# Optimization experiments

Hardware: AMD Instinct MI355X
Metric: run time of the kernel (lower is better)

## Reference

```python
import jax, jax.numpy as jnp
import numpy as np

TEMPERATURE = 0.5  # NT-Xent temperature (SimCLR default in SACLR)
NEG_INF = -1e9


def ntxent(zi, zj, temperature=TEMPERATURE):
    """SimCLR NT-Xent between two views zi, zj of shape [B, D]."""
    B = zi.shape[0]
    z = jnp.concatenate([zi, zj], axis=0)                      # [2B, D]
    z = z / (jnp.linalg.norm(z, axis=1, keepdims=True) + 1e-8)  # cosine sim
    sim = (z @ z.T) / temperature                              # [2B, 2B]
    n = 2 * B
    sim = jnp.where(jnp.eye(n, dtype=bool), NEG_INF, sim)      # mask self
    labels = jnp.concatenate([jnp.arange(B) + B, jnp.arange(B)])
    logp = jax.nn.log_softmax(sim, axis=1)
    return -jnp.mean(logp[jnp.arange(n), labels])


def setup_inputs() -> dict:
    key = jax.random.key(0)
    k1, k2, k3 = jax.random.split(key, 3)
    B, D, W, H, CA = 512, 256, 14, 14, 8
    return {
        "global_feature": jax.random.normal(k1, (B, D), dtype=jnp.float32),
        "att": jax.random.uniform(k2, (B, CA, W, H), dtype=jnp.float32),
        "outputs": jax.random.normal(k3, (B, D, W, H), dtype=jnp.float32),
    }


def reference(global_feature, att, outputs):
    # attention = sum over attention-map channel, shape [B, W, H]
    attention = jnp.sum(att, axis=1)
    B, D, W, H = outputs.shape
    P = W * H
    # Flatten spatial positions in the same (i over W, j over H) row-major order
    # as the original nested python loops.
    local_feats = jnp.transpose(outputs, (2, 3, 0, 1)).reshape(P, B, D)   # [P, B, D]
    local_atts = jnp.transpose(attention, (1, 2, 0)).reshape(P, B)        # [P, B]

    # Faithful quirk of the original: global_feature is re-softmaxed at every
    # spatial position (it is reassigned inside the loop), so carry it in a scan.
    def step(g, xs):
        lf, la = xs
        g = jax.nn.softmax(g, axis=1)          # repeated softmax on global
        lf = jax.nn.softmax(lf, axis=1)        # softmax on local feature
        l = ntxent(lf, g) * jnp.mean(la) / P   # weighted NT-Xent term
        return g, l

    _, losses = jax.lax.scan(step, global_feature, (local_feats, local_atts))
    return jnp.sum(losses)
```

## Files before the change

### kernel.cpp

```cpp
#include <hip/hip_runtime.h>

#define B_   512
#define D_   256
#define P_   196
#define N2B  1024

#define CSCALE 1.69864364f
#define LN2    0.69314718f
#define T2L    2.8853900817779268f

typedef __attribute__((ext_vector_type(8))) short short8;
typedef __attribute__((ext_vector_type(4))) float f32x4;
typedef unsigned int u32;

#define LDSP(x) ((__attribute__((address_space(3))) u32*)(x))
#define GLBP(x) ((const __attribute__((address_space(1))) u32*)(x))

__device__ unsigned short g_Z[(size_t)P_ * N2B * D_];
__device__ float g_rowps[(size_t)P_ * 8 * N2B];
__device__ float g_pp2[P_ * 4];
__device__ float g_mApart[128 * P_];
__device__ float g_dscale[(size_t)B_ * P_];
__device__ float g_partials[P_];

static __device__ const unsigned char TROW36[36] = {
  0,0,0,0,0,0,0,0, 1,1,1,1,1,1,1, 2,2,2,2,2,2, 3,3,3,3,3, 4,4,4,4, 5,5,5, 6,6, 7};
static __device__ const unsigned char TCOL36[36] = {
  0,1,2,3,4,5,6,7, 1,2,3,4,5,6,7, 2,3,4,5,6,7, 3,4,5,6,7, 4,5,6,7, 5,6,7, 6,7, 7};

static __device__ inline unsigned short f2bf(float f) {
    union { float f; unsigned int u; } v; v.f = f;
    unsigned int u = v.u;
    return (unsigned short)((u + 0x7fffu + ((u >> 16) & 1u)) >> 16);
}
static __device__ inline float bf2f(unsigned short h) {
    union { unsigned int u; float f; } v; v.u = ((unsigned int)h) << 16;
    return v.f;
}
static __device__ inline float wave_sum(float v) {
    for (int off = 32; off > 0; off >>= 1) v += __shfl_xor(v, off, 64);
    return v;
}

template<int CTRL>
static __device__ inline float dpp_add_step(float v) {
    int t = __builtin_amdgcn_update_dpp(0, __float_as_int(v), CTRL, 0xf, 0xf, true);
    return v + __int_as_float(t);
}
static __device__ inline float row16_sum(float v) {
    v = dpp_add_step<0xB1>(v);
    v = dpp_add_step<0x4E>(v);
    v = dpp_add_step<0x141>(v);
    v = dpp_add_step<0x140>(v);
    return v;
}

__global__ __launch_bounds__(256) void prep12_kernel(const float* __restrict__ gf,
                                                     const float* __restrict__ att,
                                                     const float* __restrict__ outs) {
    int blk = blockIdx.x, t = threadIdx.x;

    if (blk < 32) {
        int wv = t >> 6, lane = t & 63;
        int rw = lane >> 4, lr = lane & 15;
        int b = blk * 16 + wv * 4 + rw;
        const float4* gfr = (const float4*)(gf + (size_t)b * D_);
        float g[16], e[16];
        {
            float4 q0 = gfr[lr], q1 = gfr[lr + 16], q2 = gfr[lr + 32], q3 = gfr[lr + 48];
            g[0]=q0.x; g[1]=q0.y; g[2]=q0.z; g[3]=q0.w;
            g[4]=q1.x; g[5]=q1.y; g[6]=q1.z; g[7]=q1.w;
            g[8]=q2.x; g[9]=q2.y; g[10]=q2.z; g[11]=q2.w;
            g[12]=q3.x; g[13]=q3.y; g[14]=q3.z; g[15]=q3.w;
        }
        for (int p = 0; p < P_; ++p) {
            float s1 = 0.0f, s2 = 0.0f;
#pragma unroll
            for (int i = 0; i < 16; ++i) {
                e[i] = __expf(g[i]);
                s1 += e[i];
                s2 = fmaf(e[i], e[i], s2);
            }
            s1 = row16_sum(s1);
            s2 = row16_sum(s2);
            float isq = rsqrtf(s2) * CSCALE;
            float inv = 1.0f / s1;
            unsigned short* zr = g_Z + ((size_t)p * N2B + B_ + b) * D_;
#pragma unroll
            for (int c = 0; c < 4; ++c) {
                ushort4 o;
                o.x = f2bf(e[c * 4 + 0] * isq);
                o.y = f2bf(e[c * 4 + 1] * isq);
                o.z = f2bf(e[c * 4 + 2] * isq);
                o.w = f2bf(e[c * 4 + 3] * isq);
                *(ushort4*)(zr + c * 64 + lr * 4) = o;
            }
#pragma unroll
            for (int i = 0; i < 16; ++i) g[i] = e[i] * inv;
        }
    } else if (blk < 544) {
        int b = blk - 32;
        if (t < P_) {
            const float* src = outs + (size_t)b * (D_ * P_) + t;
            float s = 0.0f;
#pragma unroll 8
            for (int d = 0; d < 256; ++d) s += exp2f(src[(size_t)d * P_] * T2L);
            g_dscale[(size_t)b * P_ + t] = rsqrtf(s) * CSCALE;
        }
    } else {
        int bk = blk - 544;
        if (t < P_) {
            float acc = 0.0f;
            const float* base = att + (size_t)bk * 32 * P_ + t;
            for (int r = 0; r < 32; ++r) acc += base[(size_t)r * P_];
            g_mApart[bk * P_ + t] = acc;
        }
    }
}

__global__ __launch_bounds__(256) void prep2_kernel(const float* __restrict__ outs) {
    __shared__ unsigned short vt[128 * 202];
    __shared__ float ss[P_];
    int blk = blockIdx.x, t = threadIdx.x;
    int b = blk >> 1, dh = blk & 1;
    const float4* src4 = (const float4*)(outs + (size_t)b * (D_ * P_) + dh * (128 * P_));
    for (int idx = t; idx < 6272; idx += 256) {
        int d = idx / 49, c = idx - d * 49;
        float4 v = src4[idx];
        unsigned short* dst = vt + d * 202 + c * 4;
        ushort2 a, bb;
        a.x = f2bf(v.x); a.y = f2bf(v.y); bb.x = f2bf(v.z); bb.y = f2bf(v.w);
        *(ushort2*)dst = a; *(ushort2*)(dst + 2) = bb;
    }
    if (t < P_) ss[t] = g_dscale[(size_t)b * P_ + t];
    __syncthreads();
    int w = t >> 6, l = t & 63;
    for (int i = 0; i < 49; ++i) {
        int p = w * 49 + i;
        float v0 = bf2f(vt[(2 * l) * 202 + p]);
        float v1 = bf2f(vt[(2 * l + 1) * 202 + p]);
        float sc = ss[p];
        ushort2 o;
        o.x = f2bf(__expf(v0) * sc);
        o.y = f2bf(__expf(v1) * sc);
        *(ushort2*)(g_Z + ((size_t)p * N2B + b) * D_ + dh * 128 + 2 * l) = o;
    }
}

template<int MODE>
static __device__ inline void do_epi(const f32x4 acc[4][4], float psum[4][4], float pcs[4],
                                     float& pp, int wdiag, int lr, int r4) {
#pragma unroll
    for (int i = 0; i < 4; ++i) {
#pragma unroll
        for (int j = 0; j < 4; ++j) {
#pragma unroll
            for (int r = 0; r < 4; ++r) {
                float a = acc[i][j][r];
                float e = exp2f(a);
                if (MODE == 1) {
                    if (wdiag && i == j) e = (r4 + r == lr) ? 0.0f : e;
                }
                psum[i][r] += e;
                pcs[j] += e;
                if (MODE == 2) {
                    if (wdiag && i == j && (r4 + r == lr)) pp += a * LN2;
                }
            }
        }
    }
}

__global__ __launch_bounds__(256, 4) void sim_kernel() {
    __shared__ __align__(16) unsigned short As[128 * 64];
    __shared__ __align__(16) unsigned short Bs[128 * 64];
    __shared__ float combuf[512];
    __shared__ float ppred[4];

    int lin0 = blockIdx.x;
    int xcd = lin0 & 7, slot = lin0 >> 3;
    int lin = xcd * 882 + slot;
    int p = lin / 36;
    int t36 = lin - p * 36;
    int trow = TROW36[t36], tcol = TCOL36[t36];
    bool DIAG = (trow == tcol);
    bool PART = (trow < 4) && (tcol == trow + 4);

    int tid = threadIdx.x;
    int wv = tid >> 6, lane = tid & 63;
    int wr = wv >> 1, wc = wv & 1;
    int lr = lane & 15;
    int lk16 = (lane >> 4) * 16;
    bool skipw = DIAG && (wv == 2);

    const char* zb = (const char*)g_Z + (size_t)p * ((size_t)N2B * D_ * 2);
    const char* gA = zb + (size_t)trow * (128 * 512);
    const char* gB = zb + (size_t)tcol * (128 * 512);
    int lsub = (lane >> 3) * 512 + (((lane & 7) ^ (lane >> 3)) << 4);

    f32x4 acc[4][4];
#pragma unroll
    for (int i = 0; i < 4; ++i)
#pragma unroll
        for (int j = 0; j < 4; ++j)
            acc[i][j] = (f32x4){0.0f, 0.0f, 0.0f, 0.0f};

    const char* BsR = DIAG ? (const char*)As : (const char*)Bs;

    for (int ko = 0; ko < 4; ++ko) {
#pragma unroll
        for (int it = 0; it < 4; ++it) {
            int s = it * 4 + wv;
            int go = s * 4096 + ko * 128 + lsub;
            __builtin_amdgcn_global_load_lds(GLBP(gA + go), LDSP((char*)As + s * 1024), 16, 0, 0);
            if (!DIAG)
                __builtin_amdgcn_global_load_lds(GLBP(gB + go), LDSP((char*)Bs + s * 1024), 16, 0, 0);
        }
        __syncthreads();
        if (!skipw) {
#pragma unroll
            for (int ks = 0; ks < 2; ++ks) {
                int kswz = (ks * 64 + lk16) ^ ((lr & 7) << 4);
                short8 a[4], b[4];
#pragma unroll
                for (int i = 0; i < 4; ++i) {
                    a[i] = *(const short8*)((const char*)As + (wr * 64 + i * 16 + lr) * 128 + kswz);
                    b[i] = *(const short8*)(BsR + (wc * 64 + i * 16 + lr) * 128 + kswz);
                }
#pragma unroll
                for (int i = 0; i < 4; ++i)
#pragma unroll
                    for (int j = 0; j < 4; ++j)
                        acc[i][j] = __builtin_amdgcn_mfma_f32_16x16x32_bf16(a[i], b[j], acc[i][j], 0, 0, 0);
            }
        }
        __syncthreads();
    }

    int wdiag = (wr == wc);
    int r4 = (lane >> 4) * 4;
    float psum[4][4];
    float pcs[4] = {0.0f, 0.0f, 0.0f, 0.0f};
    float pp = 0.0f;
#pragma unroll
    for (int i = 0; i < 4; ++i)
#pragma unroll
        for (int r = 0; r < 4; ++r) psum[i][r] = 0.0f;

    if (!skipw) {
        if (DIAG)      do_epi<1>(acc, psum, pcs, pp, wdiag, lr, r4);
        else if (PART) do_epi<2>(acc, psum, pcs, pp, wdiag, lr, r4);
        else           do_epi<0>(acc, psum, pcs, pp, wdiag, lr, r4);
    }

    float* rowbuf = combuf;
    float* colbuf = combuf + 256;
    if (!skipw) {
#pragma unroll
        for (int i = 0; i < 4; ++i)
#pragma unroll
            for (int r = 0; r < 4; ++r) {
                float ps = psum[i][r];
                ps += __shfl_xor(ps, 1, 64);
                ps += __shfl_xor(ps, 2, 64);
                ps += __shfl_xor(ps, 4, 64);
                ps += __shfl_xor(ps, 8, 64);
                if (lr == 0) rowbuf[wc * 128 + wr * 64 + i * 16 + r4 + r] = ps;
            }
    }
    if (!DIAG) {
#pragma unroll
        for (int j = 0; j < 4; ++j) {
            float pc = pcs[j];
            pc += __shfl_xor(pc, 16, 64);
            pc += __shfl_xor(pc, 32, 64);
            if (lane < 16) colbuf[wr * 128 + wc * 64 + j * 16 + lane] = pc;
        }
    } else if (wv == 1) {
#pragma unroll
        for (int j = 0; j < 4; ++j) {
            float pc = pcs[j];
            pc += __shfl_xor(pc, 16, 64);
            pc += __shfl_xor(pc, 32, 64);
            if (lane < 16) rowbuf[64 + j * 16 + lane] = pc;
        }
    }
    if (PART) {
        float pw = wave_sum(pp);
        if (lane == 0) ppred[wv] = pw;
    }
    __syncthreads();

    if (tid < 128) {
        float v = rowbuf[tid] + rowbuf[128 + tid];
        g_rowps[((size_t)p * 8 + tcol) * N2B + trow * 128 + tid] = v;
    } else if (!DIAG) {
        int x = tid - 128;
        float v = colbuf[x] + colbuf[128 + x];
        g_rowps[((size_t)p * 8 + trow) * N2B + tcol * 128 + x] = v;
    }
    if (PART && tid == 0)
        g_pp2[p * 4 + trow] = 2.0f * (ppred[0] + ppred[1] + ppred[2] + ppred[3]);
}

__global__ __launch_bounds__(256) void rowreduce_kernel() {
    int p = blockIdx.x, t = threadIdx.x;
    const float* base = g_rowps + (size_t)p * 8 * N2B;
    float s = 0.0f;
    for (int r = t; r < N2B; r += 256) {
        float S = 0.0f;
#pragma unroll
        for (int k = 0; k < 8; ++k) S += base[(size_t)k * N2B + r];
        s += __logf(S);
    }
    s = wave_sum(s);
    __shared__ float red[4];
    int wv = t >> 6, lane = t & 63;
    if (lane == 0) red[wv] = s;
    __syncthreads();
    if (t == 0) {
        float tot = red[0] + red[1] + red[2] + red[3];
        float pp = g_pp2[p * 4 + 0] + g_pp2[p * 4 + 1] + g_pp2[p * 4 + 2] + g_pp2[p * 4 + 3];
        float ma = 0.0f;
        for (int k = 0; k < 128; ++k) ma += g_mApart[k * P_ + p];
        g_partials[p] = (tot - pp) * (ma * (1.0f / B_));
    }
}

__global__ __launch_bounds__(256) void final_kernel(float* __restrict__ out) {
    int t = threadIdx.x;
    float s = (t < P_) ? g_partials[t] : 0.0f;
    s = wave_sum(s);
    __shared__ float red[4];
    int wv = t >> 6, lane = t & 63;
    if (lane == 0) red[wv] = s;
    __syncthreads();
    if (t == 0) out[0] = (red[0] + red[1] + red[2] + red[3]) * (1.0f / ((float)N2B * (float)P_));
}

extern "C" void kernel_launch(void* const* d_in, const int* in_sizes, int n_in,
                              void* d_out, int out_size, void* d_ws, size_t ws_size,
                              hipStream_t stream) {
    const float* gf   = (const float*)d_in[0];
    const float* att  = (const float*)d_in[1];
    const float* outs = (const float*)d_in[2];
    float* out = (float*)d_out;

    hipLaunchKernelGGL(prep12_kernel, dim3(672), dim3(256), 0, stream, gf, att, outs);
    hipLaunchKernelGGL(prep2_kernel, dim3(B_ * 2), dim3(256), 0, stream, outs);
    hipLaunchKernelGGL(sim_kernel, dim3(P_ * 36), dim3(256), 0, stream);
    hipLaunchKernelGGL(rowreduce_kernel, dim3(P_), dim3(256), 0, stream);
    hipLaunchKernelGGL(final_kernel, dim3(1), dim3(256), 0, stream, out);
}
```

Measured before the change: 353.8 us.

## Double-buffer LDS tiles in sim kernel and parallelize attention-mean reduction

Splits the sim kernel's K loop into a two-stage LDS double buffer. Global-to-LDS loads for step k+2 are issued while MFMAs consume step k, with explicit vmcnt waits and barriers, and occupancy is lowered to 2 blocks per CU to fit the doubled shared memory. Diagonal tiles now load B into their own buffer as well, which adds redundant traffic. Separately, the rowreduce kernel replaces a 128-iteration serial loop on thread 0 with a wave-level parallel sum.

```diff
diff --git a/kernel.cpp b/kernel.cpp
--- a/kernel.cpp
+++ b/kernel.cpp
@@ -171,9 +171,9 @@
     }
 }
 
-__global__ __launch_bounds__(256, 4) void sim_kernel() {
-    __shared__ __align__(16) unsigned short As[128 * 64];
-    __shared__ __align__(16) unsigned short Bs[128 * 64];
+__global__ __launch_bounds__(256, 2) void sim_kernel() {
+    __shared__ __align__(16) unsigned short As[2][8192];
+    __shared__ __align__(16) unsigned short Bs[2][8192];
     __shared__ float combuf[512];
     __shared__ float ppred[4];
 
@@ -205,37 +205,57 @@
         for (int j = 0; j < 4; ++j)
             acc[i][j] = (f32x4){0.0f, 0.0f, 0.0f, 0.0f};
 
-    const char* BsR = DIAG ? (const char*)As : (const char*)Bs;
-
-    for (int ko = 0; ko < 4; ++ko) {
-#pragma unroll
-        for (int it = 0; it < 4; ++it) {
-            int s = it * 4 + wv;
-            int go = s * 4096 + ko * 128 + lsub;
-            __builtin_amdgcn_global_load_lds(GLBP(gA + go), LDSP((char*)As + s * 1024), 16, 0, 0);
-            if (!DIAG)
-                __builtin_amdgcn_global_load_lds(GLBP(gB + go), LDSP((char*)Bs + s * 1024), 16, 0, 0);
-        }
-        __syncthreads();
-        if (!skipw) {
-#pragma unroll
-            for (int ks = 0; ks < 2; ++ks) {
-                int kswz = (ks * 64 + lk16) ^ ((lr & 7) << 4);
-                short8 a[4], b[4];
-#pragma unroll
-                for (int i = 0; i < 4; ++i) {
-                    a[i] = *(const short8*)((const char*)As + (wr * 64 + i * 16 + lr) * 128 + kswz);
-                    b[i] = *(const short8*)(BsR + (wc * 64 + i * 16 + lr) * 128 + kswz);
-                }
-#pragma unroll
-                for (int i = 0; i < 4; ++i)
-#pragma unroll
-                    for (int j = 0; j < 4; ++j)
-                        acc[i][j] = __builtin_amdgcn_mfma_f32_16x16x32_bf16(a[i], b[j], acc[i][j], 0, 0, 0);
-            }
-        }
-        __syncthreads();
-    }
+#define STAGE(KO, BUF) \
+    _Pragma("unroll") \
+    for (int it = 0; it < 4; ++it) { \
+        int s = it * 4 + wv; \
+        int go = s * 4096 + (KO) * 128 + lsub; \
+        __builtin_amdgcn_global_load_lds(GLBP(gA + go), LDSP((char*)As[BUF] + s * 1024), 16, 0, 0); \
+        __builtin_amdgcn_global_load_lds(GLBP(gB + go), LDSP((char*)Bs[BUF] + s * 1024), 16, 0, 0); \
+    }
+
+    STAGE(0, 0)
+    STAGE(1, 1)
+
+#define SIM_ITER(KO, VMS) { \
+    asm volatile("s_waitcnt vmcnt(" VMS ")" ::: "memory"); \
+    __builtin_amdgcn_sched_barrier(0); \
+    __builtin_amdgcn_s_barrier(); \
+    __builtin_amdgcn_sched_barrier(0); \
+    short8 a[2][4], b[2][4]; \
+    if (!skipw) { \
+        _Pragma("unroll") \
+        for (int ks = 0; ks < 2; ++ks) { \
+            int kswz = (ks * 64 + lk16) ^ ((lr & 7) << 4); \
+            _Pragma("unroll") \
+            for (int i = 0; i < 4; ++i) { \
+                a[ks][i] = *(const short8*)((const char*)As[(KO) & 1] + (wr * 64 + i * 16 + lr) * 128 + kswz); \
+                b[ks][i] = *(const short8*)((const char*)Bs[(KO) & 1] + (wc * 64 + i * 16 + lr) * 128 + kswz); \
+            } \
+        } \
+    } \
+    asm volatile("s_waitcnt lgkmcnt(0)" ::: "memory"); \
+    __builtin_amdgcn_sched_barrier(0); \
+    __builtin_amdgcn_s_barrier(); \
+    __builtin_amdgcn_sched_barrier(0); \
+    if ((KO) + 2 < 4) { STAGE((KO) + 2, (KO) & 1) } \
+    if (!skipw) { \
+        _Pragma("unroll") \
+        for (int ks = 0; ks < 2; ++ks) \
+            _Pragma("unroll") \
+            for (int i = 0; i < 4; ++i) \
+                _Pragma("unroll") \
+                for (int j = 0; j < 4; ++j) \
+                    acc[i][j] = __builtin_amdgcn_mfma_f32_16x16x32_bf16(a[ks][i], b[ks][j], acc[i][j], 0, 0, 0); \
+    } \
+}
+
+    SIM_ITER(0, "8")
+    SIM_ITER(1, "8")
+    SIM_ITER(2, "8")
+    SIM_ITER(3, "0")
+#undef SIM_ITER
+#undef STAGE
 
     int wdiag = (wr == wc);
     int r4 = (lane >> 4) * 4;
@@ -314,15 +334,16 @@
         s += __logf(S);
     }
     s = wave_sum(s);
-    __shared__ float red[4];
+    float mp = (t < 128) ? g_mApart[t * P_ + p] : 0.0f;
+    mp = wave_sum(mp);
+    __shared__ float red[4], redm[4];
     int wv = t >> 6, lane = t & 63;
-    if (lane == 0) red[wv] = s;
+    if (lane == 0) { red[wv] = s; redm[wv] = mp; }
     __syncthreads();
     if (t == 0) {
         float tot = red[0] + red[1] + red[2] + red[3];
         float pp = g_pp2[p * 4 + 0] + g_pp2[p * 4 + 1] + g_pp2[p * 4 + 2] + g_pp2[p * 4 + 3];
-        float ma = 0.0f;
-        for (int k = 0; k < 128; ++k) ma += g_mApart[k * P_ + p];
+        float ma = redm[0] + redm[1];
         g_partials[p] = (tot - pp) * (ma * (1.0f / B_));
     }
 }
```

Measured after the change: 366.2 us. +3.5%, slower.
